# Kernel optimization log

Measured on AMD Instinct MI355X. Metric: run time of the kernel, lower is better.

The kernel has to match this reference:

```python
import jax, jax.numpy as jnp
import numpy as np

N_ASSETS = 512
WINDOW = 256
BATCH = 32
THRESHOLDS = (0.3, 0.5, 0.7)
N_SQUARINGS = 9  # ceil(log2(N_ASSETS)); reachability converges after log2(n) squarings


def setup_inputs() -> dict:
    key = jax.random.key(0)
    returns = jax.random.normal(key, (BATCH, WINDOW, N_ASSETS), dtype=jnp.float32)
    return {"returns": returns}


def _betti_features(corr):
    """corr: (B, N, N). Returns (B, 2*len(THRESHOLDS)) Betti features."""
    B, N, _ = corr.shape
    eye = jnp.eye(N, dtype=jnp.float32)
    idx = jnp.arange(N)
    feats = []
    for t in THRESHOLDS:
        # adjacency with zeroed diagonal (matches np.fill_diagonal(adj, 0))
        adj = (jnp.abs(corr) > t).astype(jnp.float32) * (1.0 - eye)
        # transitive closure via repeated boolean squaring of (A | I)
        R = jnp.minimum(adj + eye, 1.0)
        for _ in range(N_SQUARINGS):
            R = (jnp.einsum('bij,bjk->bik', R, R) > 0).astype(jnp.float32)
        # component representative of node i = smallest reachable index;
        # number of components = count of self-representatives
        comp_rep = jnp.argmax(R, axis=-1)              # first 1 along row = min index
        components = jnp.sum(comp_rep == idx[None, :], axis=-1).astype(jnp.float32)
        edges = jnp.sum(adj, axis=(-1, -2)) / 2.0
        betti0 = components
        betti1 = jnp.maximum(0.0, edges - N + components)
        feats.append(betti0 / N)
        feats.append(betti1 / N)
    return jnp.stack(feats, axis=-1)  # (B, 2*n_thresholds), order [t0_b0, t0_b1, t1_b0, ...]


def reference(returns) -> jnp.ndarray:
    B, W, N = returns.shape
    ret_centered = returns - returns.mean(axis=1, keepdims=True)
    # torch .std() is unbiased (ddof=1)
    std = jnp.std(ret_centered, axis=1, keepdims=True, ddof=1) + 1e-8
    ret_normalized = ret_centered / std
    corr = jnp.einsum('bwi,bwj->bij', ret_normalized, ret_normalized) / W
    return _betti_features(corr)
```

## Files before the change

kernel.cpp:

```cpp
#include <hip/hip_runtime.h>
#include <hip/hip_bf16.h>
#include <stdint.h>

#define NASSETS 512
#define WINDOW  256
#define NBATCH  32
#define NWORDS  16
#define BM 128
#define BN 128

typedef __attribute__((ext_vector_type(4))) float floatx4;
typedef __attribute__((ext_vector_type(4))) int   intx4;
typedef __attribute__((ext_vector_type(2))) long  longx2;

__device__ __forceinline__ unsigned int f2e4m3_manual(float x) {
    union { float f; unsigned u; } c; c.f = x;
    unsigned s = (c.u >> 24) & 0x80u;
    unsigned a = c.u & 0x7FFFFFFFu;
    float af = fabsf(x);
    unsigned code;
    if (af >= 448.f) code = 0x7Eu;
    else if (af < 0.015625f) {
        code = (unsigned)(int)rintf(af * 512.f);
    } else {
        unsigned E = a >> 23;
        unsigned base = ((E - 120u) << 3) | ((a >> 20) & 7u);
        unsigned rem = a & 0xFFFFFu;
        if (rem > 0x80000u || (rem == 0x80000u && (base & 1u))) base++;
        if (base > 0x7Eu) base = 0x7Eu;
        code = base;
    }
    return s | code;
}

__device__ __forceinline__ int pack4fp8(float f0, float f1, float f2, float f3) {
#if defined(__has_builtin) && __has_builtin(__builtin_amdgcn_cvt_pk_fp8_f32)
    int v = 0;
    v = __builtin_amdgcn_cvt_pk_fp8_f32(f0, f1, v, false);
    v = __builtin_amdgcn_cvt_pk_fp8_f32(f2, f3, v, true);
    return v;
#else
    return (int)(f2e4m3_manual(f0) | (f2e4m3_manual(f1) << 8) |
                 (f2e4m3_manual(f2) << 16) | (f2e4m3_manual(f3) << 24));
#endif
}

__device__ __forceinline__ void gload16(const void* gp, void* lp) {
    __builtin_amdgcn_global_load_lds(
        (const __attribute__((address_space(1))) void*)(uintptr_t)gp,
        (__attribute__((address_space(3))) void*)(unsigned int)(uintptr_t)lp,
        16, 0, 0);
}

__global__ __launch_bounds__(512)
void normalize_kernel(const float* __restrict__ ret, char* __restrict__ Xt) {
    __shared__ float sred[512];
    __shared__ float ssred[512];
    __shared__ float smean[64];
    __shared__ float sinv[64];
    __shared__ __align__(16) char tile[64 * 256];

    const int t  = threadIdx.x;
    const int a  = t & 63;
    const int wc = t >> 6;
    const int g  = blockIdx.x;
    const int b  = blockIdx.y;
    const int n0 = g * 64;

    const float* base = ret + (size_t)b * WINDOW * NASSETS + n0 + a;

    float x[32];
    float s1 = 0.f, s2 = 0.f;
#pragma unroll
    for (int k = 0; k < 32; ++k) {
        x[k] = base[(size_t)(wc * 32 + k) * NASSETS];
        s1 += x[k];
        s2 += x[k] * x[k];
    }
    sred[wc * 64 + a]  = s1;
    ssred[wc * 64 + a] = s2;
    __syncthreads();

    if (t < 64) {
        float S = 0.f, S2 = 0.f;
#pragma unroll
        for (int c = 0; c < 8; ++c) { S += sred[c * 64 + t]; S2 += ssred[c * 64 + t]; }
        float mean = S / (float)WINDOW;
        float var  = (S2 - (float)WINDOW * mean * mean) / (float)(WINDOW - 1);
        if (var < 0.f) var = 0.f;
        float stdv = sqrtf(var) + 1e-8f;
        smean[t] = mean;
        sinv[t]  = 1.0f / stdv;
    }
    __syncthreads();

    const float mn = smean[a];
    const float iv = sinv[a];

    int pk[8];
#pragma unroll
    for (int j = 0; j < 8; ++j)
        pk[j] = pack4fp8((x[4*j+0] - mn) * iv, (x[4*j+1] - mn) * iv,
                         (x[4*j+2] - mn) * iv, (x[4*j+3] - mn) * iv);

    char* rowp = tile + a * 256;
    const int s  = wc >> 1;
    const int h8 = (wc & 1) * 8;
#pragma unroll
    for (int q = 0; q < 4; ++q) {
        unsigned long long piece = (unsigned)pk[2*q] |
                                   ((unsigned long long)(unsigned)pk[2*q+1] << 32);
        int L = s * 4 + q;
        *(unsigned long long*)(rowp + ((L ^ (a & 15)) * 16) + h8) = piece;
    }
    __syncthreads();

    char* orow = Xt + ((size_t)b * NASSETS + n0) * WINDOW;
#pragma unroll
    for (int it = 0; it < 2; ++it) {
        int idx = it * 512 + t;
        int r = idx >> 4;
        int sl = idx & 15;
        intx4 v = *(const intx4*)(tile + r * 256 + ((sl ^ (r & 15)) * 16));
        *(intx4*)(orow + r * WINDOW + sl * 16) = v;
    }
}

__global__ __launch_bounds__(256)
void corr_adj_kernel(const char* __restrict__ Xt, unsigned int* __restrict__ adj) {
    __shared__ __align__(16) char lsA[BM * 64];
    __shared__ __align__(16) char lsB[BN * 64];

    const int t    = threadIdx.x;
    const int lane = t & 63;
    const int wave = t >> 6;
    const int wi   = wave >> 1, wj = wave & 1;
    const int b  = blockIdx.z;
    const int i0 = blockIdx.y * BM;
    const int j0 = blockIdx.x * BN;

    const char* base = Xt + (size_t)b * NASSETS * WINDOW;

    const int m  = lane & 15;
    const int kq = lane >> 4;

    const int srowAdd  = lane >> 2;
    const int gslotOff = ((lane & 3) ^ ((lane >> 2) & 3)) * 16;

    floatx4 acc[4][4] = {};

    for (int k0 = 0; k0 < WINDOW; k0 += 64) {
        __syncthreads();
#pragma unroll
        for (int c = 0; c < 2; ++c) {
            int r0 = (wave * 2 + c) * 16;
            const char* gA = base + (size_t)(i0 + r0 + srowAdd) * WINDOW + k0 + gslotOff;
            const char* gB = base + (size_t)(j0 + r0 + srowAdd) * WINDOW + k0 + gslotOff;
            gload16(gA, (char*)lsA + r0 * 64);
            gload16(gB, (char*)lsB + r0 * 64);
        }
        __syncthreads();

        longx2 af[4], bf[4];
#pragma unroll
        for (int mi = 0; mi < 4; ++mi) {
            int r = wi * 64 + mi * 16 + m;
            af[mi] = *(const longx2*)(lsA + r * 64 + ((kq ^ (r & 3)) * 16));
        }
#pragma unroll
        for (int nj = 0; nj < 4; ++nj) {
            int r = wj * 64 + nj * 16 + m;
            bf[nj] = *(const longx2*)(lsB + r * 64 + ((kq ^ (r & 3)) * 16));
        }
#pragma unroll
        for (int mi = 0; mi < 4; ++mi)
#pragma unroll
            for (int nj = 0; nj < 4; ++nj) {
                acc[mi][nj] = __builtin_amdgcn_mfma_f32_16x16x32_fp8_fp8(
                    af[mi].x, bf[nj].x, acc[mi][nj], 0, 0, 0);
                acc[mi][nj] = __builtin_amdgcn_mfma_f32_16x16x32_fp8_fp8(
                    af[mi].y, bf[nj].y, acc[mi][nj], 0, 0, 0);
            }
    }

    const float T[3] = {0.3f * (float)WINDOW, 0.5f * (float)WINDOW, 0.7f * (float)WINDOW};
    unsigned int wout[3][2] = {{0u,0u},{0u,0u},{0u,0u}};
    const int qp = (lane >> 2) & 3;
#pragma unroll
    for (int mi = 0; mi < 4; ++mi) {
#pragma unroll
        for (int r = 0; r < 4; ++r) {
            bool act = ((lane >> 4) == mi) && ((lane & 3) == r);
#pragma unroll
            for (int th = 0; th < 3; ++th) {
                unsigned long long b0 = __ballot(fabsf(acc[mi][0][r]) > T[th]);
                unsigned long long b1 = __ballot(fabsf(acc[mi][1][r]) > T[th]);
                unsigned long long b2 = __ballot(fabsf(acc[mi][2][r]) > T[th]);
                unsigned long long b3 = __ballot(fabsf(acc[mi][3][r]) > T[th]);
                if (act) {
                    wout[th][0] = ((unsigned)(b0 >> (qp * 16)) & 0xFFFFu)
                                | (((unsigned)(b1 >> (qp * 16)) & 0xFFFFu) << 16);
                    wout[th][1] = ((unsigned)(b2 >> (qp * 16)) & 0xFFFFu)
                                | (((unsigned)(b3 >> (qp * 16)) & 0xFFFFu) << 16);
                }
            }
        }
    }

    const int grow    = i0 + wi * 64 + lane;
    const int colbase = j0 + wj * 64;
    unsigned int dd = (unsigned int)(grow - colbase);
    if (dd < 64u) {
        unsigned int m0 = (dd < 32u) ? ~(1u << dd) : 0xFFFFFFFFu;
        unsigned int m1 = (dd >= 32u) ? ~(1u << (dd - 32u)) : 0xFFFFFFFFu;
#pragma unroll
        for (int th = 0; th < 3; ++th) { wout[th][0] &= m0; wout[th][1] &= m1; }
    }
    const int wb = colbase >> 5;
    const size_t stride_t = (size_t)NBATCH * NASSETS * NWORDS;
    size_t rb = ((size_t)b * NASSETS + grow) * NWORDS + wb;
#pragma unroll
    for (int th = 0; th < 3; ++th) {
        adj[rb + th * stride_t]     = wout[th][0];
        adj[rb + th * stride_t + 1] = wout[th][1];
    }
}

__global__ __launch_bounds__(512)
void betti_kernel(const unsigned int* __restrict__ adj, float* __restrict__ out) {
    __shared__ int lab[NASSETS];
    __shared__ int changed;
    __shared__ int red[8];

    int th = blockIdx.x;
    int b  = blockIdx.y;
    int i  = threadIdx.x;
    int lane = i & 63, wv = i >> 6;

    const unsigned int* rowp =
        adj + (((size_t)th * NBATCH + b) * NASSETS + i) * NWORDS;
    unsigned int row[NWORDS];
    int deg = 0;
#pragma unroll
    for (int w = 0; w < NWORDS; ++w) {
        row[w] = rowp[w];
        deg += __popc(row[w]);
    }

    int v = deg;
#pragma unroll
    for (int off = 32; off > 0; off >>= 1) v += __shfl_down(v, off);
    if (lane == 0) red[wv] = v;
    lab[i] = i;
    __syncthreads();
    int total_deg = 0;
    if (i == 0)
        for (int k = 0; k < 8; ++k) total_deg += red[k];

    for (;;) {
        __syncthreads();
        if (i == 0) changed = 0;
        __syncthreads();
        int mlab = lab[i];
#pragma unroll
        for (int w = 0; w < NWORDS; ++w) {
            unsigned int bits = row[w];
            int basej = w * 32;
            while (bits) {
                int j = basej + __builtin_ctz(bits);
                bits &= bits - 1;
                int lj = lab[j];
                if (lj < mlab) mlab = lj;
            }
        }
        int lm = lab[mlab];
        if (lm < mlab) mlab = lm;
        __syncthreads();
        if (mlab < lab[i]) { lab[i] = mlab; changed = 1; }
        __syncthreads();
        if (!changed) break;
    }

    int isrep = (lab[i] == i) ? 1 : 0;
#pragma unroll
    for (int off = 32; off > 0; off >>= 1) isrep += __shfl_down(isrep, off);
    if (lane == 0) red[wv] = isrep;
    __syncthreads();
    if (i == 0) {
        int comps = 0;
        for (int k = 0; k < 8; ++k) comps += red[k];
        float compf = (float)comps;
        float edges = (float)total_deg * 0.5f;
        out[b * 6 + th * 2 + 0] = compf / (float)NASSETS;
        out[b * 6 + th * 2 + 1] = fmaxf(0.0f, edges - (float)NASSETS + compf) / (float)NASSETS;
    }
}

extern "C" void kernel_launch(void* const* d_in, const int* in_sizes, int n_in,
                              void* d_out, int out_size, void* d_ws, size_t ws_size,
                              hipStream_t stream) {
    const float* ret = (const float*)d_in[0];
    float* out = (float*)d_out;
    char* ws = (char*)d_ws;

    char* Xt = ws;
    unsigned int* adj =
        (unsigned int*)(ws + (size_t)NBATCH * NASSETS * WINDOW);

    dim3 g1(NASSETS / 64, NBATCH);
    normalize_kernel<<<g1, 512, 0, stream>>>(ret, Xt);

    dim3 g2(NASSETS / BN, NASSETS / BM, NBATCH);
    corr_adj_kernel<<<g2, 256, 0, stream>>>(Xt, adj);

    dim3 g3(3, NBATCH);
    betti_kernel<<<g3, 512, 0, stream>>>(adj, out);
}
```

Baseline: 78.45 us.

## Fuse normalize, correlation and Betti kernels into one persistent kernel with grid barriers

New measurement: 219.8 us. 180% more time.

```diff
diff --git a/kernel.cpp b/kernel.cpp
--- a/kernel.cpp
+++ b/kernel.cpp
@@ -6,8 +6,7 @@
 #define WINDOW  256
 #define NBATCH  32
 #define NWORDS  16
-#define BM 128
-#define BN 128
+#define NBLK    512
 
 typedef __attribute__((ext_vector_type(4))) float floatx4;
 typedef __attribute__((ext_vector_type(4))) int   intx4;
@@ -52,247 +51,277 @@
         16, 0, 0);
 }
 
-__global__ __launch_bounds__(512)
-void normalize_kernel(const float* __restrict__ ret, char* __restrict__ Xt) {
-    __shared__ float sred[512];
-    __shared__ float ssred[512];
-    __shared__ float smean[64];
-    __shared__ float sinv[64];
-    __shared__ __align__(16) char tile[64 * 256];
-
-    const int t  = threadIdx.x;
-    const int a  = t & 63;
-    const int wc = t >> 6;
-    const int g  = blockIdx.x;
-    const int b  = blockIdx.y;
-    const int n0 = g * 64;
-
-    const float* base = ret + (size_t)b * WINDOW * NASSETS + n0 + a;
-
-    float x[32];
-    float s1 = 0.f, s2 = 0.f;
-#pragma unroll
-    for (int k = 0; k < 32; ++k) {
-        x[k] = base[(size_t)(wc * 32 + k) * NASSETS];
-        s1 += x[k];
-        s2 += x[k] * x[k];
-    }
-    sred[wc * 64 + a]  = s1;
-    ssred[wc * 64 + a] = s2;
-    __syncthreads();
-
-    if (t < 64) {
-        float S = 0.f, S2 = 0.f;
-#pragma unroll
-        for (int c = 0; c < 8; ++c) { S += sred[c * 64 + t]; S2 += ssred[c * 64 + t]; }
-        float mean = S / (float)WINDOW;
-        float var  = (S2 - (float)WINDOW * mean * mean) / (float)(WINDOW - 1);
-        if (var < 0.f) var = 0.f;
-        float stdv = sqrtf(var) + 1e-8f;
-        smean[t] = mean;
-        sinv[t]  = 1.0f / stdv;
-    }
-    __syncthreads();
-
-    const float mn = smean[a];
-    const float iv = sinv[a];
-
-    int pk[8];
-#pragma unroll
-    for (int j = 0; j < 8; ++j)
-        pk[j] = pack4fp8((x[4*j+0] - mn) * iv, (x[4*j+1] - mn) * iv,
-                         (x[4*j+2] - mn) * iv, (x[4*j+3] - mn) * iv);
-
-    char* rowp = tile + a * 256;
-    const int s  = wc >> 1;
-    const int h8 = (wc & 1) * 8;
-#pragma unroll
-    for (int q = 0; q < 4; ++q) {
-        unsigned long long piece = (unsigned)pk[2*q] |
-                                   ((unsigned long long)(unsigned)pk[2*q+1] << 32);
-        int L = s * 4 + q;
-        *(unsigned long long*)(rowp + ((L ^ (a & 15)) * 16) + h8) = piece;
-    }
-    __syncthreads();
-
-    char* orow = Xt + ((size_t)b * NASSETS + n0) * WINDOW;
-#pragma unroll
-    for (int it = 0; it < 2; ++it) {
-        int idx = it * 512 + t;
-        int r = idx >> 4;
-        int sl = idx & 15;
-        intx4 v = *(const intx4*)(tile + r * 256 + ((sl ^ (r & 15)) * 16));
-        *(intx4*)(orow + r * WINDOW + sl * 16) = v;
-    }
-}
-
-__global__ __launch_bounds__(256)
-void corr_adj_kernel(const char* __restrict__ Xt, unsigned int* __restrict__ adj) {
-    __shared__ __align__(16) char lsA[BM * 64];
-    __shared__ __align__(16) char lsB[BN * 64];
+__global__ __launch_bounds__(256, 2)
+void fused_topo_kernel(const float* __restrict__ ret, char* __restrict__ Xt,
+                       unsigned int* __restrict__ adj, int* __restrict__ bar,
+                       float* __restrict__ out) {
+    __shared__ __align__(16) char smem[16384];
+    __shared__ float sred[256];
+    __shared__ float ssred[256];
+    __shared__ float smean[32];
+    __shared__ float sinv[32];
+    __shared__ int lab[NASSETS];
+    __shared__ int red[8];
+    __shared__ int changed;
 
     const int t    = threadIdx.x;
+    const int blk  = blockIdx.x;
     const int lane = t & 63;
     const int wave = t >> 6;
-    const int wi   = wave >> 1, wj = wave & 1;
-    const int b  = blockIdx.z;
-    const int i0 = blockIdx.y * BM;
-    const int j0 = blockIdx.x * BN;
-
-    const char* base = Xt + (size_t)b * NASSETS * WINDOW;
-
-    const int m  = lane & 15;
-    const int kq = lane >> 4;
-
-    const int srowAdd  = lane >> 2;
-    const int gslotOff = ((lane & 3) ^ ((lane >> 2) & 3)) * 16;
-
-    floatx4 acc[4][4] = {};
-
-    for (int k0 = 0; k0 < WINDOW; k0 += 64) {
-        __syncthreads();
-#pragma unroll
-        for (int c = 0; c < 2; ++c) {
-            int r0 = (wave * 2 + c) * 16;
-            const char* gA = base + (size_t)(i0 + r0 + srowAdd) * WINDOW + k0 + gslotOff;
-            const char* gB = base + (size_t)(j0 + r0 + srowAdd) * WINDOW + k0 + gslotOff;
-            gload16(gA, (char*)lsA + r0 * 64);
-            gload16(gB, (char*)lsB + r0 * 64);
-        }
-        __syncthreads();
-
-        longx2 af[4], bf[4];
+
+    {
+        const int a  = t & 31;
+        const int wc = t >> 5;
+        const int b  = blk >> 4;
+        const int n0 = (blk & 15) * 32;
+        const float* col = ret + (size_t)b * WINDOW * NASSETS + n0 + a;
+
+        float x[32];
+        float s1 = 0.f, s2 = 0.f;
+#pragma unroll
+        for (int k = 0; k < 32; ++k) {
+            x[k] = col[(size_t)(wc * 32 + k) * NASSETS];
+            s1 += x[k];
+            s2 += x[k] * x[k];
+        }
+        sred[wc * 32 + a]  = s1;
+        ssred[wc * 32 + a] = s2;
+        __syncthreads();
+
+        if (t < 32) {
+            float S = 0.f, S2 = 0.f;
+#pragma unroll
+            for (int c = 0; c < 8; ++c) { S += sred[c * 32 + t]; S2 += ssred[c * 32 + t]; }
+            float mean = S / (float)WINDOW;
+            float var  = (S2 - (float)WINDOW * mean * mean) / (float)(WINDOW - 1);
+            if (var < 0.f) var = 0.f;
+            float stdv = sqrtf(var) + 1e-8f;
+            smean[t] = mean;
+            sinv[t]  = 1.0f / stdv;
+        }
+        __syncthreads();
+
+        const float mn = smean[a];
+        const float iv = sinv[a];
+
+        int pk[8];
+#pragma unroll
+        for (int j = 0; j < 8; ++j)
+            pk[j] = pack4fp8((x[4*j+0] - mn) * iv, (x[4*j+1] - mn) * iv,
+                             (x[4*j+2] - mn) * iv, (x[4*j+3] - mn) * iv);
+
+        char* rowp = smem + a * 256;
+        const int s  = wc >> 1;
+        const int h8 = (wc & 1) * 8;
+#pragma unroll
+        for (int q = 0; q < 4; ++q) {
+            unsigned long long piece = (unsigned)pk[2*q] |
+                                       ((unsigned long long)(unsigned)pk[2*q+1] << 32);
+            int L = s * 4 + q;
+            *(unsigned long long*)(rowp + ((L ^ (a & 15)) * 16) + h8) = piece;
+        }
+        __syncthreads();
+
+        char* orow = Xt + ((size_t)b * NASSETS + n0) * WINDOW;
+#pragma unroll
+        for (int it = 0; it < 2; ++it) {
+            int idx = it * 256 + t;
+            int r  = idx >> 4;
+            int sl = idx & 15;
+            intx4 v = *(const intx4*)(smem + r * 256 + ((sl ^ (r & 15)) * 16));
+            *(intx4*)(orow + r * WINDOW + sl * 16) = v;
+        }
+    }
+
+    __syncthreads();
+    if (t == 0) {
+        __threadfence();
+        __hip_atomic_fetch_add(&bar[0], 1, __ATOMIC_RELEASE, __HIP_MEMORY_SCOPE_AGENT);
+        while (__hip_atomic_load(&bar[0], __ATOMIC_ACQUIRE, __HIP_MEMORY_SCOPE_AGENT) < NBLK)
+            __builtin_amdgcn_s_sleep(2);
+        __threadfence();
+    }
+    __syncthreads();
+
+    {
+        char* lsA = smem;
+        char* lsB = smem + 8192;
+        const int b  = blk >> 4;
+        const int it = (blk >> 2) & 3;
+        const int jt = blk & 3;
+        const int i0 = it * 128;
+        const int j0 = jt * 128;
+        const int wi = wave >> 1, wj = wave & 1;
+
+        const char* base = Xt + (size_t)b * NASSETS * WINDOW;
+        const int m  = lane & 15;
+        const int kq = lane >> 4;
+        const int srowAdd  = lane >> 2;
+        const int gslotOff = ((lane & 3) ^ ((lane >> 2) & 3)) * 16;
+
+        floatx4 acc[4][4] = {};
+
+        for (int k0 = 0; k0 < WINDOW; k0 += 64) {
+            __syncthreads();
+#pragma unroll
+            for (int c = 0; c < 2; ++c) {
+                int r0 = (wave * 2 + c) * 16;
+                const char* gA = base + (size_t)(i0 + r0 + srowAdd) * WINDOW + k0 + gslotOff;
+                const char* gB = base + (size_t)(j0 + r0 + srowAdd) * WINDOW + k0 + gslotOff;
+                gload16(gA, lsA + r0 * 64);
+                gload16(gB, lsB + r0 * 64);
+            }
+            __syncthreads();
+
+            longx2 af[4], bf[4];
+#pragma unroll
+            for (int mi = 0; mi < 4; ++mi) {
+                int r = wi * 64 + mi * 16 + m;
+                af[mi] = *(const longx2*)(lsA + r * 64 + ((kq ^ (r & 3)) * 16));
+            }
+#pragma unroll
+            for (int nj = 0; nj < 4; ++nj) {
+                int r = wj * 64 + nj * 16 + m;
+                bf[nj] = *(const longx2*)(lsB + r * 64 + ((kq ^ (r & 3)) * 16));
+            }
+#pragma unroll
+            for (int mi = 0; mi < 4; ++mi)
+#pragma unroll
+                for (int nj = 0; nj < 4; ++nj) {
+                    acc[mi][nj] = __builtin_amdgcn_mfma_f32_16x16x32_fp8_fp8(
+                        af[mi].x, bf[nj].x, acc[mi][nj], 0, 0, 0);
+                    acc[mi][nj] = __builtin_amdgcn_mfma_f32_16x16x32_fp8_fp8(
+                        af[mi].y, bf[nj].y, acc[mi][nj], 0, 0, 0);
+                }
+        }
+
+        const float T[3] = {0.3f * (float)WINDOW, 0.5f * (float)WINDOW, 0.7f * (float)WINDOW};
+        unsigned int wout[3][2] = {{0u,0u},{0u,0u},{0u,0u}};
+        const int qp = (lane >> 2) & 3;
 #pragma unroll
         for (int mi = 0; mi < 4; ++mi) {
-            int r = wi * 64 + mi * 16 + m;
-            af[mi] = *(const longx2*)(lsA + r * 64 + ((kq ^ (r & 3)) * 16));
-        }
-#pragma unroll
-        for (int nj = 0; nj < 4; ++nj) {
-            int r = wj * 64 + nj * 16 + m;
-            bf[nj] = *(const longx2*)(lsB + r * 64 + ((kq ^ (r & 3)) * 16));
-        }
-#pragma unroll
-        for (int mi = 0; mi < 4; ++mi)
-#pragma unroll
-            for (int nj = 0; nj < 4; ++nj) {
-                acc[mi][nj] = __builtin_amdgcn_mfma_f32_16x16x32_fp8_fp8(
-                    af[mi].x, bf[nj].x, acc[mi][nj], 0, 0, 0);
-                acc[mi][nj] = __builtin_amdgcn_mfma_f32_16x16x32_fp8_fp8(
-                    af[mi].y, bf[nj].y, acc[mi][nj], 0, 0, 0);
-            }
-    }
-
-    const float T[3] = {0.3f * (float)WINDOW, 0.5f * (float)WINDOW, 0.7f * (float)WINDOW};
-    unsigned int wout[3][2] = {{0u,0u},{0u,0u},{0u,0u}};
-    const int qp = (lane >> 2) & 3;
-#pragma unroll
-    for (int mi = 0; mi < 4; ++mi) {
-#pragma unroll
-        for (int r = 0; r < 4; ++r) {
-            bool act = ((lane >> 4) == mi) && ((lane & 3) == r);
-#pragma unroll
-            for (int th = 0; th < 3; ++th) {
-                unsigned long long b0 = __ballot(fabsf(acc[mi][0][r]) > T[th]);
-                unsigned long long b1 = __ballot(fabsf(acc[mi][1][r]) > T[th]);
-                unsigned long long b2 = __ballot(fabsf(acc[mi][2][r]) > T[th]);
-                unsigned long long b3 = __ballot(fabsf(acc[mi][3][r]) > T[th]);
-                if (act) {
-                    wout[th][0] = ((unsigned)(b0 >> (qp * 16)) & 0xFFFFu)
-                                | (((unsigned)(b1 >> (qp * 16)) & 0xFFFFu) << 16);
-                    wout[th][1] = ((unsigned)(b2 >> (qp * 16)) & 0xFFFFu)
-                                | (((unsigned)(b3 >> (qp * 16)) & 0xFFFFu) << 16);
+#pragma unroll
+            for (int r = 0; r < 4; ++r) {
+                bool act = ((lane >> 4) == mi) && ((lane & 3) == r);
+#pragma unroll
+                for (int th = 0; th < 3; ++th) {
+                    unsigned long long b0 = __ballot(fabsf(acc[mi][0][r]) > T[th]);
+                    unsigned long long b1 = __ballot(fabsf(acc[mi][1][r]) > T[th]);
+                    unsigned long long b2 = __ballot(fabsf(acc[mi][2][r]) > T[th]);
+                    unsigned long long b3 = __ballot(fabsf(acc[mi][3][r]) > T[th]);
+                    if (act) {
+                        wout[th][0] = ((unsigned)(b0 >> (qp * 16)) & 0xFFFFu)
+                                    | (((unsigned)(b1 >> (qp * 16)) & 0xFFFFu) << 16);
+                        wout[th][1] = ((unsigned)(b2 >> (qp * 16)) & 0xFFFFu)
+                                    | (((unsigned)(b3 >> (qp * 16)) & 0xFFFFu) << 16);
+                    }
                 }
             }
         }
-    }
-
-    const int grow    = i0 + wi * 64 + lane;
-    const int colbase = j0 + wj * 64;
-    unsigned int dd = (unsigned int)(grow - colbase);
-    if (dd < 64u) {
-        unsigned int m0 = (dd < 32u) ? ~(1u << dd) : 0xFFFFFFFFu;
-        unsigned int m1 = (dd >= 32u) ? ~(1u << (dd - 32u)) : 0xFFFFFFFFu;
-#pragma unroll
-        for (int th = 0; th < 3; ++th) { wout[th][0] &= m0; wout[th][1] &= m1; }
-    }
-    const int wb = colbase >> 5;
-    const size_t stride_t = (size_t)NBATCH * NASSETS * NWORDS;
-    size_t rb = ((size_t)b * NASSETS + grow) * NWORDS + wb;
-#pragma unroll
-    for (int th = 0; th < 3; ++th) {
-        adj[rb + th * stride_t]     = wout[th][0];
-        adj[rb + th * stride_t + 1] = wout[th][1];
-    }
-}
-
-__global__ __launch_bounds__(512)
-void betti_kernel(const unsigned int* __restrict__ adj, float* __restrict__ out) {
-    __shared__ int lab[NASSETS];
-    __shared__ int changed;
-    __shared__ int red[8];
-
-    int th = blockIdx.x;
-    int b  = blockIdx.y;
-    int i  = threadIdx.x;
-    int lane = i & 63, wv = i >> 6;
-
-    const unsigned int* rowp =
-        adj + (((size_t)th * NBATCH + b) * NASSETS + i) * NWORDS;
-    unsigned int row[NWORDS];
-    int deg = 0;
-#pragma unroll
-    for (int w = 0; w < NWORDS; ++w) {
-        row[w] = rowp[w];
-        deg += __popc(row[w]);
-    }
-
-    int v = deg;
-#pragma unroll
-    for (int off = 32; off > 0; off >>= 1) v += __shfl_down(v, off);
-    if (lane == 0) red[wv] = v;
-    lab[i] = i;
+
+        const int grow    = i0 + wi * 64 + lane;
+        const int colbase = j0 + wj * 64;
+        unsigned int dd = (unsigned int)(grow - colbase);
+        if (dd < 64u) {
+            unsigned int m0 = (dd < 32u) ? ~(1u << dd) : 0xFFFFFFFFu;
+            unsigned int m1 = (dd >= 32u) ? ~(1u << (dd - 32u)) : 0xFFFFFFFFu;
+#pragma unroll
+            for (int th = 0; th < 3; ++th) { wout[th][0] &= m0; wout[th][1] &= m1; }
+        }
+        const int wb = colbase >> 5;
+        const size_t stride_t = (size_t)NBATCH * NASSETS * NWORDS;
+        size_t rb = ((size_t)b * NASSETS + grow) * NWORDS + wb;
+#pragma unroll
+        for (int th = 0; th < 3; ++th) {
+            adj[rb + th * stride_t]     = wout[th][0];
+            adj[rb + th * stride_t + 1] = wout[th][1];
+        }
+    }
+
     __syncthreads();
-    int total_deg = 0;
-    if (i == 0)
-        for (int k = 0; k < 8; ++k) total_deg += red[k];
-
-    for (;;) {
-        __syncthreads();
-        if (i == 0) changed = 0;
-        __syncthreads();
-        int mlab = lab[i];
+    if (t == 0) {
+        __threadfence();
+        __hip_atomic_fetch_add(&bar[1], 1, __ATOMIC_RELEASE, __HIP_MEMORY_SCOPE_AGENT);
+        while (__hip_atomic_load(&bar[1], __ATOMIC_ACQUIRE, __HIP_MEMORY_SCOPE_AGENT) < NBLK)
+            __builtin_amdgcn_s_sleep(2);
+        __threadfence();
+    }
+    __syncthreads();
+
+    if (blk < 3 * NBATCH) {
+        const int th = blk >> 5;
+        const int b  = blk & 31;
+        const int n1 = t + 256;
+
+        const unsigned int* rp =
+            adj + (((size_t)th * NBATCH + b) * NASSETS + t) * NWORDS;
+        unsigned int rowA[NWORDS], rowB[NWORDS];
+        int deg = 0;
 #pragma unroll
         for (int w = 0; w < NWORDS; ++w) {
-            unsigned int bits = row[w];
-            int basej = w * 32;
-            while (bits) {
-                int j = basej + __builtin_ctz(bits);
-                bits &= bits - 1;
-                int lj = lab[j];
-                if (lj < mlab) mlab = lj;
-            }
-        }
-        int lm = lab[mlab];
-        if (lm < mlab) mlab = lm;
-        __syncthreads();
-        if (mlab < lab[i]) { lab[i] = mlab; changed = 1; }
-        __syncthreads();
-        if (!changed) break;
-    }
-
-    int isrep = (lab[i] == i) ? 1 : 0;
-#pragma unroll
-    for (int off = 32; off > 0; off >>= 1) isrep += __shfl_down(isrep, off);
-    if (lane == 0) red[wv] = isrep;
-    __syncthreads();
-    if (i == 0) {
-        int comps = 0;
-        for (int k = 0; k < 8; ++k) comps += red[k];
-        float compf = (float)comps;
-        float edges = (float)total_deg * 0.5f;
-        out[b * 6 + th * 2 + 0] = compf / (float)NASSETS;
-        out[b * 6 + th * 2 + 1] = fmaxf(0.0f, edges - (float)NASSETS + compf) / (float)NASSETS;
+            rowA[w] = rp[w];
+            rowB[w] = rp[256 * NWORDS + w];
+            deg += __popc(rowA[w]) + __popc(rowB[w]);
+        }
+
+        int v = deg;
+#pragma unroll
+        for (int off = 32; off > 0; off >>= 1) v += __shfl_down(v, off);
+        if (lane == 0) red[wave] = v;
+        lab[t]  = t;
+        lab[n1] = n1;
+        __syncthreads();
+        int total_deg = 0;
+        if (t == 0)
+            for (int k = 0; k < 4; ++k) total_deg += red[k];
+
+        for (;;) {
+            __syncthreads();
+            if (t == 0) changed = 0;
+            __syncthreads();
+            int m0 = lab[t];
+            int m1 = lab[n1];
+#pragma unroll
+            for (int w = 0; w < NWORDS; ++w) {
+                unsigned int bits = rowA[w];
+                int basej = w * 32;
+                while (bits) {
+                    int j = basej + __builtin_ctz(bits);
+                    bits &= bits - 1;
+                    int lj = lab[j];
+                    if (lj < m0) m0 = lj;
+                }
+                bits = rowB[w];
+                while (bits) {
+                    int j = basej + __builtin_ctz(bits);
+                    bits &= bits - 1;
+                    int lj = lab[j];
+                    if (lj < m1) m1 = lj;
+                }
+            }
+            int lm0 = lab[m0]; if (lm0 < m0) m0 = lm0;
+            int lm1 = lab[m1]; if (lm1 < m1) m1 = lm1;
+            __syncthreads();
+            if (m0 < lab[t])  { lab[t]  = m0; changed = 1; }
+            if (m1 < lab[n1]) { lab[n1] = m1; changed = 1; }
+            __syncthreads();
+            if (!changed) break;
+        }
+
+        int isrep = ((lab[t] == t) ? 1 : 0) + ((lab[n1] == n1) ? 1 : 0);
+#pragma unroll
+        for (int off = 32; off > 0; off >>= 1) isrep += __shfl_down(isrep, off);
+        __syncthreads();
+        if (lane == 0) red[wave] = isrep;
+        __syncthreads();
+        if (t == 0) {
+            int comps = 0;
+            for (int k = 0; k < 4; ++k) comps += red[k];
+            float compf = (float)comps;
+            float edges = (float)total_deg * 0.5f;
+            out[b * 6 + th * 2 + 0] = compf / (float)NASSETS;
+            out[b * 6 + th * 2 + 1] = fmaxf(0.0f, edges - (float)NASSETS + compf) / (float)NASSETS;
+        }
     }
 }
 
@@ -306,13 +335,8 @@
     char* Xt = ws;
     unsigned int* adj =
         (unsigned int*)(ws + (size_t)NBATCH * NASSETS * WINDOW);
-
-    dim3 g1(NASSETS / 64, NBATCH);
-    normalize_kernel<<<g1, 512, 0, stream>>>(ret, Xt);
-
-    dim3 g2(NASSETS / BN, NASSETS / BM, NBATCH);
-    corr_adj_kernel<<<g2, 256, 0, stream>>>(Xt, adj);
-
-    dim3 g3(3, NBATCH);
-    betti_kernel<<<g3, 512, 0, stream>>>(adj, out);
-}
+    int* bar = (int*)(ws + (8u << 20));
+
+    hipMemsetAsync(bar, 0, 2 * sizeof(int), stream);
+    fused_topo_kernel<<<NBLK, 256, 0, stream>>>(ret, Xt, adj, bar, out);
+}
```

## Fuse connected-components pass into correlation kernel via last-block atomic counter

Applied to the files above, without the earlier changes.

After: 94.38 us. 1.2x slower.

```diff
diff --git a/kernel.cpp b/kernel.cpp
--- a/kernel.cpp
+++ b/kernel.cpp
@@ -119,7 +119,7 @@
 #pragma unroll
     for (int it = 0; it < 2; ++it) {
         int idx = it * 512 + t;
-        int r = idx >> 4;
+        int r  = idx >> 4;
         int sl = idx & 15;
         intx4 v = *(const intx4*)(tile + r * 256 + ((sl ^ (r & 15)) * 16));
         *(intx4*)(orow + r * WINDOW + sl * 16) = v;
@@ -127,9 +127,14 @@
 }
 
 __global__ __launch_bounds__(256)
-void corr_adj_kernel(const char* __restrict__ Xt, unsigned int* __restrict__ adj) {
+void corr_cc_kernel(const char* __restrict__ Xt, unsigned int* __restrict__ adj,
+                    int* __restrict__ cnt, float* __restrict__ out) {
     __shared__ __align__(16) char lsA[BM * 64];
     __shared__ __align__(16) char lsB[BN * 64];
+    __shared__ int lab[NASSETS];
+    __shared__ int red[4];
+    __shared__ int changed;
+    __shared__ int isLast;
 
     const int t    = threadIdx.x;
     const int lane = t & 63;
@@ -143,7 +148,6 @@
 
     const int m  = lane & 15;
     const int kq = lane >> 4;
-
     const int srowAdd  = lane >> 2;
     const int gslotOff = ((lane & 3) ^ ((lane >> 2) & 3)) * 16;
 
@@ -221,78 +225,93 @@
     size_t rb = ((size_t)b * NASSETS + grow) * NWORDS + wb;
 #pragma unroll
     for (int th = 0; th < 3; ++th) {
-        adj[rb + th * stride_t]     = wout[th][0];
-        adj[rb + th * stride_t + 1] = wout[th][1];
-    }
-}
-
-__global__ __launch_bounds__(512)
-void betti_kernel(const unsigned int* __restrict__ adj, float* __restrict__ out) {
-    __shared__ int lab[NASSETS];
-    __shared__ int changed;
-    __shared__ int red[8];
-
-    int th = blockIdx.x;
-    int b  = blockIdx.y;
-    int i  = threadIdx.x;
-    int lane = i & 63, wv = i >> 6;
-
-    const unsigned int* rowp =
-        adj + (((size_t)th * NBATCH + b) * NASSETS + i) * NWORDS;
-    unsigned int row[NWORDS];
-    int deg = 0;
-#pragma unroll
-    for (int w = 0; w < NWORDS; ++w) {
-        row[w] = rowp[w];
-        deg += __popc(row[w]);
-    }
-
-    int v = deg;
-#pragma unroll
-    for (int off = 32; off > 0; off >>= 1) v += __shfl_down(v, off);
-    if (lane == 0) red[wv] = v;
-    lab[i] = i;
-    __syncthreads();
-    int total_deg = 0;
-    if (i == 0)
-        for (int k = 0; k < 8; ++k) total_deg += red[k];
-
-    for (;;) {
-        __syncthreads();
-        if (i == 0) changed = 0;
-        __syncthreads();
-        int mlab = lab[i];
+        __hip_atomic_store(&adj[rb + th * stride_t],     wout[th][0],
+                           __ATOMIC_RELAXED, __HIP_MEMORY_SCOPE_AGENT);
+        __hip_atomic_store(&adj[rb + th * stride_t + 1], wout[th][1],
+                           __ATOMIC_RELAXED, __HIP_MEMORY_SCOPE_AGENT);
+    }
+
+    __syncthreads();
+    if (t == 0) {
+        int old = __hip_atomic_fetch_add(&cnt[b], 1, __ATOMIC_ACQ_REL,
+                                         __HIP_MEMORY_SCOPE_AGENT);
+        isLast = (old == 15) ? 1 : 0;
+    }
+    __syncthreads();
+    if (!isLast) return;
+
+    const int n1 = t + 256;
+    for (int th = 0; th < 3; ++th) {
+        __syncthreads();
+        const unsigned int* rp =
+            adj + (((size_t)th * NBATCH + b) * NASSETS + t) * NWORDS;
+        unsigned int rowA[NWORDS], rowB[NWORDS];
+        int deg = 0;
 #pragma unroll
         for (int w = 0; w < NWORDS; ++w) {
-            unsigned int bits = row[w];
-            int basej = w * 32;
-            while (bits) {
-                int j = basej + __builtin_ctz(bits);
-                bits &= bits - 1;
-                int lj = lab[j];
-                if (lj < mlab) mlab = lj;
+            rowA[w] = rp[w];
+            rowB[w] = rp[256 * NWORDS + w];
+            deg += __popc(rowA[w]) + __popc(rowB[w]);
+        }
+
+        int v = deg;
+#pragma unroll
+        for (int off = 32; off > 0; off >>= 1) v += __shfl_down(v, off);
+        if (lane == 0) red[wave] = v;
+        lab[t]  = t;
+        lab[n1] = n1;
+        __syncthreads();
+        int total_deg = 0;
+        if (t == 0)
+            for (int k = 0; k < 4; ++k) total_deg += red[k];
+
+        for (;;) {
+            __syncthreads();
+            if (t == 0) changed = 0;
+            __syncthreads();
+            int m0 = lab[t];
+            int m1 = lab[n1];
+#pragma unroll
+            for (int w = 0; w < NWORDS; ++w) {
+                unsigned int bits = rowA[w];
+                int basej = w * 32;
+                while (bits) {
+                    int j = basej + __builtin_ctz(bits);
+                    bits &= bits - 1;
+                    int lj = lab[j];
+                    if (lj < m0) m0 = lj;
+                }
+                bits = rowB[w];
+                while (bits) {
+                    int j = basej + __builtin_ctz(bits);
+                    bits &= bits - 1;
+                    int lj = lab[j];
+                    if (lj < m1) m1 = lj;
+                }
             }
-        }
-        int lm = lab[mlab];
-        if (lm < mlab) mlab = lm;
-        __syncthreads();
-        if (mlab < lab[i]) { lab[i] = mlab; changed = 1; }
-        __syncthreads();
-        if (!changed) break;
-    }
-
-    int isrep = (lab[i] == i) ? 1 : 0;
-#pragma unroll
-    for (int off = 32; off > 0; off >>= 1) isrep += __shfl_down(isrep, off);
-    if (lane == 0) red[wv] = isrep;
-    __syncthreads();
-    if (i == 0) {
-        int comps = 0;
-        for (int k = 0; k < 8; ++k) comps += red[k];
-        float compf = (float)comps;
-        float edges = (float)total_deg * 0.5f;
-        out[b * 6 + th * 2 + 0] = compf / (float)NASSETS;
-        out[b * 6 + th * 2 + 1] = fmaxf(0.0f, edges - (float)NASSETS + compf) / (float)NASSETS;
+            int lm0 = lab[m0]; if (lm0 < m0) m0 = lm0;
+            int lm1 = lab[m1]; if (lm1 < m1) m1 = lm1;
+            __syncthreads();
+            if (m0 < lab[t])  { lab[t]  = m0; changed = 1; }
+            if (m1 < lab[n1]) { lab[n1] = m1; changed = 1; }
+            __syncthreads();
+            if (!changed) break;
+        }
+
+        int isrep = ((lab[t] == t) ? 1 : 0) + ((lab[n1] == n1) ? 1 : 0);
+#pragma unroll
+        for (int off = 32; off > 0; off >>= 1) isrep += __shfl_down(isrep, off);
+        __syncthreads();
+        if (lane == 0) red[wave] = isrep;
+        __syncthreads();
+        if (t == 0) {
+            int comps = 0;
+            for (int k = 0; k < 4; ++k) comps += red[k];
+            float compf = (float)comps;
+            float edges = (float)total_deg * 0.5f;
+            out[b * 6 + th * 2 + 0] = compf / (float)NASSETS;
+            out[b * 6 + th * 2 + 1] = fmaxf(0.0f, edges - (float)NASSETS + compf) / (float)NASSETS;
+        }
     }
 }
 
@@ -306,13 +325,13 @@
     char* Xt = ws;
     unsigned int* adj =
         (unsigned int*)(ws + (size_t)NBATCH * NASSETS * WINDOW);
+    int* cnt = (int*)(ws + (8u << 20));
+
+    hipMemsetAsync(cnt, 0, NBATCH * sizeof(int), stream);
 
     dim3 g1(NASSETS / 64, NBATCH);
     normalize_kernel<<<g1, 512, 0, stream>>>(ret, Xt);
 
     dim3 g2(NASSETS / BN, NASSETS / BM, NBATCH);
-    corr_adj_kernel<<<g2, 256, 0, stream>>>(Xt, adj);
-
-    dim3 g3(3, NBATCH);
-    betti_kernel<<<g3, 512, 0, stream>>>(adj, out);
-}
+    corr_cc_kernel<<<g2, 256, 0, stream>>>(Xt, adj, cnt, out);
+}
```
